# Kernel tuning notes

Measured on AMD Instinct MI355X. Metric: run time of the kernel, lower is better.

Reference implementation:

```python
import jax, jax.numpy as jnp
import numpy as np

CLAMP_MIN = 1e-12
CLAMP_MAX = 1e12


def setup_inputs() -> dict:
    key = jax.random.key(0)
    k1, k2, k3 = jax.random.split(key, 3)
    N, C, H, W = 32, 11, 384, 384
    x = jax.random.normal(k1, (N, C, H, W), dtype=jnp.float32)
    centers = jax.random.normal(k2, (N, C, H, W), dtype=jnp.float32)
    labels = jax.random.randint(k3, (N, H, W), 0, C, dtype=jnp.int64)
    return {"x": x, "centers": centers, "labels": labels}


def reference(x, centers, labels):
    # x, centers: (N, C, H, W); labels: (N, H, W) int
    N, C, H, W = x.shape
    # res[n,c] = x[n,c]^2 + centers[n,c]^2 - 2 * x[n,c] @ centers[n,c]
    # (single batched matmul replaces the original per-(i,j) addmm loop)
    res = x * x + centers * centers - 2.0 * jnp.matmul(x, centers)
    # softmax over class dim, then max over class dim -> (N, H, W)
    res_max = jnp.max(jax.nn.softmax(res, axis=1), axis=1)
    dist = res_max * labels.astype(res_max.dtype)
    loss = jnp.sum(jnp.clip(dist, CLAMP_MIN, CLAMP_MAX)) / (H * W * N)
    return loss
```

## Files before the change

### kernel.cpp

```cpp
#include <hip/hip_runtime.h>
#include <stdint.h>

typedef __attribute__((ext_vector_type(8))) short short8;
typedef __attribute__((ext_vector_type(4))) float floatx4;
typedef __attribute__((ext_vector_type(4))) unsigned short u16x4;

#define Hh 384
#define Ww 384
#define Cc 11
#define Nn 32
#define PITCH 72

__device__ __forceinline__ unsigned short f2bf(float f) {
  union { float f; uint32_t u; } z; z.f = f;
  return (unsigned short)(z.u >> 16);
}
__device__ __forceinline__ float bf2f(unsigned short b) {
  union { uint32_t u; float f; } z; z.u = ((uint32_t)b) << 16;
  return z.f;
}

__global__ __launch_bounds__(256, 3)
void center_loss(const float* __restrict__ X, const float* __restrict__ Cen,
                 const int* __restrict__ Lab, float* __restrict__ Out) {
  __shared__ __align__(16) unsigned short Alds[64 * PITCH];
  __shared__ __align__(16) unsigned short Blds[64 * PITCH];
  __shared__ float red[4];

  const int bx = blockIdx.x;
  const int n  = bx / 36;
  const int t36 = bx - n * 36;
  const int ib = t36 / 6;
  const int jb = t36 - ib * 6;
  const int i0 = ib << 6, j0 = jb << 6;

  const int t   = threadIdx.x;
  const int l   = t & 63;
  const int w   = t >> 6;
  const int wr  = (w >> 1) << 5;
  const int wc  = (w & 1) << 5;
  const int q4  = l >> 4;
  const int l16 = l & 15;
  const int sa  = t & 15;
  const int sr  = t >> 4;

  float m[16], s[16];
#pragma unroll
  for (int i = 0; i < 16; ++i) { m[i] = -3.0e38f; s[i] = 0.0f; }

  for (int c = 0; c < Cc; ++c) {
    const float* xb = X   + (size_t)(n * Cc + c) * (Hh * Ww);
    const float* cb = Cen + (size_t)(n * Cc + c) * (Hh * Ww);

    floatx4 acc[2][2];
#pragma unroll
    for (int a = 0; a < 2; ++a)
#pragma unroll
      for (int b = 0; b < 2; ++b) acc[a][b] = (floatx4){0.f, 0.f, 0.f, 0.f};
    float ev[16];
#pragma unroll
    for (int i = 0; i < 16; ++i) ev[i] = 0.0f;

    for (int kb = 0; kb < 6; ++kb) {
      __syncthreads();
      {
        const float* ap = xb + (size_t)(i0 + sr) * Ww + (kb << 6) + (sa << 2);
#pragma unroll
        for (int p = 0; p < 4; ++p) {
          float4 v = *reinterpret_cast<const float4*>(ap + (size_t)(p * 16) * Ww);
          u16x4 pk;
          pk.x = f2bf(v.x); pk.y = f2bf(v.y); pk.z = f2bf(v.z); pk.w = f2bf(v.w);
          *reinterpret_cast<u16x4*>(&Alds[(sr + 16 * p) * PITCH + (sa << 2)]) = pk;
        }
      }
      {
#pragma unroll
        for (int p = 0; p < 2; ++p) {
          const int kbase = (w << 3) + (p << 5);
          const float* bp = cb + (size_t)((kb << 6) + kbase) * Ww + j0 + l;
          short8 pk;
#pragma unroll
          for (int u = 0; u < 8; ++u) pk[u] = (short)f2bf(bp[(size_t)u * Ww]);
          *reinterpret_cast<short8*>(&Blds[l * PITCH + kbase]) = pk;
        }
      }
      __syncthreads();

      if (kb == jb) {
#pragma unroll
        for (int fr = 0; fr < 2; ++fr)
#pragma unroll
          for (int fc = 0; fc < 2; ++fc)
#pragma unroll
            for (int r = 0; r < 4; ++r) {
              const int idx = ((fr << 1) + fc) * 4 + r;
              const int pr = wr + (fr << 4) + (q4 << 2) + r;
              const int pc = wc + (fc << 4) + l16;
              float xv = bf2f(Alds[pr * PITCH + pc]);
              ev[idx] += xv * xv;
            }
      }
      if (kb == ib) {
#pragma unroll
        for (int fr = 0; fr < 2; ++fr)
#pragma unroll
          for (int fc = 0; fc < 2; ++fc)
#pragma unroll
            for (int r = 0; r < 4; ++r) {
              const int idx = ((fr << 1) + fc) * 4 + r;
              const int pr = wr + (fr << 4) + (q4 << 2) + r;
              const int pc = wc + (fc << 4) + l16;
              float cv = bf2f(Blds[pc * PITCH + pr]);
              ev[idx] += cv * cv;
            }
      }

#pragma unroll
      for (int ks = 0; ks < 2; ++ks) {
        const int ko = (ks << 5) + (q4 << 3);
        short8 a0 = *reinterpret_cast<const short8*>(&Alds[(wr +      l16) * PITCH + ko]);
        short8 a1 = *reinterpret_cast<const short8*>(&Alds[(wr + 16 + l16) * PITCH + ko]);
        short8 b0 = *reinterpret_cast<const short8*>(&Blds[(wc +      l16) * PITCH + ko]);
        short8 b1 = *reinterpret_cast<const short8*>(&Blds[(wc + 16 + l16) * PITCH + ko]);
        acc[0][0] = __builtin_amdgcn_mfma_f32_16x16x32_bf16(a0, b0, acc[0][0], 0, 0, 0);
        acc[0][1] = __builtin_amdgcn_mfma_f32_16x16x32_bf16(a0, b1, acc[0][1], 0, 0, 0);
        acc[1][0] = __builtin_amdgcn_mfma_f32_16x16x32_bf16(a1, b0, acc[1][0], 0, 0, 0);
        acc[1][1] = __builtin_amdgcn_mfma_f32_16x16x32_bf16(a1, b1, acc[1][1], 0, 0, 0);
      }
    }

#pragma unroll
    for (int fr = 0; fr < 2; ++fr)
#pragma unroll
      for (int fc = 0; fc < 2; ++fc)
#pragma unroll
        for (int r = 0; r < 4; ++r) {
          const int idx = ((fr << 1) + fc) * 4 + r;
          float res = ev[idx] - 2.0f * acc[fr][fc][r];
          float mi = m[idx];
          if (res <= mi) {
            s[idx] += __expf(res - mi);
          } else {
            s[idx] = s[idx] * __expf(mi - res) + 1.0f;
            m[idx] = res;
          }
        }
  }

  float local = 0.0f;
  const int* lb = Lab + (size_t)n * (Hh * Ww);
#pragma unroll
  for (int fr = 0; fr < 2; ++fr)
#pragma unroll
    for (int fc = 0; fc < 2; ++fc)
#pragma unroll
      for (int r = 0; r < 4; ++r) {
        const int idx = ((fr << 1) + fc) * 4 + r;
        const int pr = i0 + wr + (fr << 4) + (q4 << 2) + r;
        const int pc = j0 + wc + (fc << 4) + l16;
        float val = 1.0f / s[idx];
        float d = val * (float)lb[pr * Ww + pc];
        d = fminf(fmaxf(d, 1e-12f), 1e12f);
        local += d;
      }
#pragma unroll
  for (int off = 32; off > 0; off >>= 1) local += __shfl_down(local, off, 64);
  if (l == 0) red[w] = local;
  __syncthreads();
  if (t == 0) {
    float bs = (red[0] + red[1] + red[2] + red[3]) * (1.0f / 4718592.0f);
    atomicAdd(Out, bs);
  }
}

extern "C" void kernel_launch(void* const* d_in, const int* in_sizes, int n_in,
                              void* d_out, int out_size, void* d_ws, size_t ws_size,
                              hipStream_t stream) {
  const float* X   = (const float*)d_in[0];
  const float* Cen = (const float*)d_in[1];
  const int*   Lab = (const int*)d_in[2];
  float* Out = (float*)d_out;
  hipMemsetAsync(Out, 0, (size_t)out_size * sizeof(float), stream);
  hipLaunchKernelGGL(center_loss, dim3(Nn * 36), dim3(256), 0, stream,
                     X, Cen, Lab, Out);
}
```

Before: 601.6 us.

## Prefetch next k-tile into registers and remap blocks by XCD

Flattens the channel and k-block loops into one 66-iteration loop. The global loads for the next tile are issued into registers before the compute on the current LDS tile, so memory latency overlaps with MFMA work. Block indices are remapped so that all blocks of one batch item land on the same XCD, which should improve L2 reuse of shared rows and columns. Launch bounds are raised to 4 waves per SIMD. The extra prefetch registers may cause spills or cut real occupancy.

```diff
diff --git a/kernel.cpp b/kernel.cpp
--- a/kernel.cpp
+++ b/kernel.cpp
@@ -20,16 +20,19 @@
   return z.f;
 }
 
-__global__ __launch_bounds__(256, 3)
+__global__ __launch_bounds__(256, 4)
 void center_loss(const float* __restrict__ X, const float* __restrict__ Cen,
                  const int* __restrict__ Lab, float* __restrict__ Out) {
   __shared__ __align__(16) unsigned short Alds[64 * PITCH];
   __shared__ __align__(16) unsigned short Blds[64 * PITCH];
   __shared__ float red[4];
 
-  const int bx = blockIdx.x;
-  const int n  = bx / 36;
-  const int t36 = bx - n * 36;
+  const int bx   = blockIdx.x;
+  const int xcd  = bx & 7;
+  const int slot = bx >> 3;
+  const int grp  = slot / 36;
+  const int t36  = slot - grp * 36;
+  const int n    = xcd + (grp << 3);
   const int ib = t36 / 6;
   const int jb = t36 - ib * 6;
   const int i0 = ib << 6, j0 = jb << 6;
@@ -44,111 +47,154 @@
   const int sa  = t & 15;
   const int sr  = t >> 4;
 
+  const size_t plane = (size_t)Hh * Ww;
+  const float* xbase = X   + (size_t)n * Cc * plane;
+  const float* cbase = Cen + (size_t)n * Cc * plane;
+
   float m[16], s[16];
 #pragma unroll
   for (int i = 0; i < 16; ++i) { m[i] = -3.0e38f; s[i] = 0.0f; }
 
-  for (int c = 0; c < Cc; ++c) {
-    const float* xb = X   + (size_t)(n * Cc + c) * (Hh * Ww);
-    const float* cb = Cen + (size_t)(n * Cc + c) * (Hh * Ww);
-
-    floatx4 acc[2][2];
-#pragma unroll
-    for (int a = 0; a < 2; ++a)
-#pragma unroll
-      for (int b = 0; b < 2; ++b) acc[a][b] = (floatx4){0.f, 0.f, 0.f, 0.f};
-    float ev[16];
-#pragma unroll
-    for (int i = 0; i < 16; ++i) ev[i] = 0.0f;
-
-    for (int kb = 0; kb < 6; ++kb) {
-      __syncthreads();
-      {
-        const float* ap = xb + (size_t)(i0 + sr) * Ww + (kb << 6) + (sa << 2);
-#pragma unroll
-        for (int p = 0; p < 4; ++p) {
-          float4 v = *reinterpret_cast<const float4*>(ap + (size_t)(p * 16) * Ww);
-          u16x4 pk;
-          pk.x = f2bf(v.x); pk.y = f2bf(v.y); pk.z = f2bf(v.z); pk.w = f2bf(v.w);
-          *reinterpret_cast<u16x4*>(&Alds[(sr + 16 * p) * PITCH + (sa << 2)]) = pk;
-        }
+  floatx4 acc[2][2];
+  float ev[16];
+#pragma unroll
+  for (int a = 0; a < 2; ++a)
+#pragma unroll
+    for (int b = 0; b < 2; ++b) acc[a][b] = (floatx4){0.f, 0.f, 0.f, 0.f};
+#pragma unroll
+  for (int i = 0; i < 16; ++i) ev[i] = 0.0f;
+
+  float4 pa[4];
+  float  pb[16];
+
+  {
+    const float* ap = xbase + (size_t)(i0 + sr) * Ww + (sa << 2);
+#pragma unroll
+    for (int p = 0; p < 4; ++p)
+      pa[p] = *reinterpret_cast<const float4*>(ap + (size_t)(p * 16) * Ww);
+#pragma unroll
+    for (int p = 0; p < 2; ++p) {
+      const int kbase = (w << 3) + (p << 5);
+      const float* bp = cbase + (size_t)kbase * Ww + j0 + l;
+#pragma unroll
+      for (int u = 0; u < 8; ++u) pb[p * 8 + u] = bp[(size_t)u * Ww];
+    }
+  }
+
+  int c = 0, kb = 0;
+  for (int it = 0; it < 66; ++it) {
+    __syncthreads();
+
+#pragma unroll
+    for (int p = 0; p < 4; ++p) {
+      u16x4 pk;
+      pk.x = f2bf(pa[p].x); pk.y = f2bf(pa[p].y);
+      pk.z = f2bf(pa[p].z); pk.w = f2bf(pa[p].w);
+      *reinterpret_cast<u16x4*>(&Alds[(sr + 16 * p) * PITCH + (sa << 2)]) = pk;
+    }
+#pragma unroll
+    for (int p = 0; p < 2; ++p) {
+      const int kbase = (w << 3) + (p << 5);
+      short8 pk;
+#pragma unroll
+      for (int u = 0; u < 8; ++u) pk[u] = (short)f2bf(pb[p * 8 + u]);
+      *reinterpret_cast<short8*>(&Blds[l * PITCH + kbase]) = pk;
+    }
+
+    int kn = kb + 1, cn = c;
+    if (kn == 6) { kn = 0; cn = c + 1; }
+    float4 na[4];
+    float  nb[16];
+    if (it < 65) {
+      const float* xb = xbase + (size_t)cn * plane;
+      const float* cb = cbase + (size_t)cn * plane;
+      const float* ap = xb + (size_t)(i0 + sr) * Ww + (kn << 6) + (sa << 2);
+#pragma unroll
+      for (int p = 0; p < 4; ++p)
+        na[p] = *reinterpret_cast<const float4*>(ap + (size_t)(p * 16) * Ww);
+#pragma unroll
+      for (int p = 0; p < 2; ++p) {
+        const int kbase = (w << 3) + (p << 5);
+        const float* bp = cb + (size_t)((kn << 6) + kbase) * Ww + j0 + l;
+#pragma unroll
+        for (int u = 0; u < 8; ++u) nb[p * 8 + u] = bp[(size_t)u * Ww];
       }
-      {
-#pragma unroll
-        for (int p = 0; p < 2; ++p) {
-          const int kbase = (w << 3) + (p << 5);
-          const float* bp = cb + (size_t)((kb << 6) + kbase) * Ww + j0 + l;
-          short8 pk;
-#pragma unroll
-          for (int u = 0; u < 8; ++u) pk[u] = (short)f2bf(bp[(size_t)u * Ww]);
-          *reinterpret_cast<short8*>(&Blds[l * PITCH + kbase]) = pk;
-        }
-      }
-      __syncthreads();
-
-      if (kb == jb) {
-#pragma unroll
-        for (int fr = 0; fr < 2; ++fr)
-#pragma unroll
-          for (int fc = 0; fc < 2; ++fc)
-#pragma unroll
-            for (int r = 0; r < 4; ++r) {
-              const int idx = ((fr << 1) + fc) * 4 + r;
-              const int pr = wr + (fr << 4) + (q4 << 2) + r;
-              const int pc = wc + (fc << 4) + l16;
-              float xv = bf2f(Alds[pr * PITCH + pc]);
-              ev[idx] += xv * xv;
+    }
+
+    __syncthreads();
+
+    if (kb == jb) {
+#pragma unroll
+      for (int fr = 0; fr < 2; ++fr)
+#pragma unroll
+        for (int fc = 0; fc < 2; ++fc)
+#pragma unroll
+          for (int r = 0; r < 4; ++r) {
+            const int idx = ((fr << 1) + fc) * 4 + r;
+            const int pr = wr + (fr << 4) + (q4 << 2) + r;
+            const int pc = wc + (fc << 4) + l16;
+            float xv = bf2f(Alds[pr * PITCH + pc]);
+            ev[idx] += xv * xv;
+          }
+    }
+    if (kb == ib) {
+#pragma unroll
+      for (int fr = 0; fr < 2; ++fr)
+#pragma unroll
+        for (int fc = 0; fc < 2; ++fc)
+#pragma unroll
+          for (int r = 0; r < 4; ++r) {
+            const int idx = ((fr << 1) + fc) * 4 + r;
+            const int pr = wr + (fr << 4) + (q4 << 2) + r;
+            const int pc = wc + (fc << 4) + l16;
+            float cv = bf2f(Blds[pc * PITCH + pr]);
+            ev[idx] += cv * cv;
+          }
+    }
+
+#pragma unroll
+    for (int ks = 0; ks < 2; ++ks) {
+      const int ko = (ks << 5) + (q4 << 3);
+      short8 a0 = *reinterpret_cast<const short8*>(&Alds[(wr +      l16) * PITCH + ko]);
+      short8 a1 = *reinterpret_cast<const short8*>(&Alds[(wr + 16 + l16) * PITCH + ko]);
+      short8 b0 = *reinterpret_cast<const short8*>(&Blds[(wc +      l16) * PITCH + ko]);
+      short8 b1 = *reinterpret_cast<const short8*>(&Blds[(wc + 16 + l16) * PITCH + ko]);
+      acc[0][0] = __builtin_amdgcn_mfma_f32_16x16x32_bf16(a0, b0, acc[0][0], 0, 0, 0);
+      acc[0][1] = __builtin_amdgcn_mfma_f32_16x16x32_bf16(a0, b1, acc[0][1], 0, 0, 0);
+      acc[1][0] = __builtin_amdgcn_mfma_f32_16x16x32_bf16(a1, b0, acc[1][0], 0, 0, 0);
+      acc[1][1] = __builtin_amdgcn_mfma_f32_16x16x32_bf16(a1, b1, acc[1][1], 0, 0, 0);
+    }
+
+    if (kb == 5) {
+#pragma unroll
+      for (int fr = 0; fr < 2; ++fr)
+#pragma unroll
+        for (int fc = 0; fc < 2; ++fc)
+#pragma unroll
+          for (int r = 0; r < 4; ++r) {
+            const int idx = ((fr << 1) + fc) * 4 + r;
+            float res = ev[idx] - 2.0f * acc[fr][fc][r];
+            float mi = m[idx];
+            if (res <= mi) {
+              s[idx] += __expf(res - mi);
+            } else {
+              s[idx] = s[idx] * __expf(mi - res) + 1.0f;
+              m[idx] = res;
             }
-      }
-      if (kb == ib) {
-#pragma unroll
-        for (int fr = 0; fr < 2; ++fr)
-#pragma unroll
-          for (int fc = 0; fc < 2; ++fc)
-#pragma unroll
-            for (int r = 0; r < 4; ++r) {
-              const int idx = ((fr << 1) + fc) * 4 + r;
-              const int pr = wr + (fr << 4) + (q4 << 2) + r;
-              const int pc = wc + (fc << 4) + l16;
-              float cv = bf2f(Blds[pc * PITCH + pr]);
-              ev[idx] += cv * cv;
-            }
-      }
-
-#pragma unroll
-      for (int ks = 0; ks < 2; ++ks) {
-        const int ko = (ks << 5) + (q4 << 3);
-        short8 a0 = *reinterpret_cast<const short8*>(&Alds[(wr +      l16) * PITCH + ko]);
-        short8 a1 = *reinterpret_cast<const short8*>(&Alds[(wr + 16 + l16) * PITCH + ko]);
-        short8 b0 = *reinterpret_cast<const short8*>(&Blds[(wc +      l16) * PITCH + ko]);
-        short8 b1 = *reinterpret_cast<const short8*>(&Blds[(wc + 16 + l16) * PITCH + ko]);
-        acc[0][0] = __builtin_amdgcn_mfma_f32_16x16x32_bf16(a0, b0, acc[0][0], 0, 0, 0);
-        acc[0][1] = __builtin_amdgcn_mfma_f32_16x16x32_bf16(a0, b1, acc[0][1], 0, 0, 0);
-        acc[1][0] = __builtin_amdgcn_mfma_f32_16x16x32_bf16(a1, b0, acc[1][0], 0, 0, 0);
-        acc[1][1] = __builtin_amdgcn_mfma_f32_16x16x32_bf16(a1, b1, acc[1][1], 0, 0, 0);
-      }
-    }
-
-#pragma unroll
-    for (int fr = 0; fr < 2; ++fr)
-#pragma unroll
-      for (int fc = 0; fc < 2; ++fc)
-#pragma unroll
-        for (int r = 0; r < 4; ++r) {
-          const int idx = ((fr << 1) + fc) * 4 + r;
-          float res = ev[idx] - 2.0f * acc[fr][fc][r];
-          float mi = m[idx];
-          if (res <= mi) {
-            s[idx] += __expf(res - mi);
-          } else {
-            s[idx] = s[idx] * __expf(mi - res) + 1.0f;
-            m[idx] = res;
+            acc[fr][fc][r] = 0.0f;
+            ev[idx] = 0.0f;
           }
-        }
+    }
+
+    kb = kn; c = cn;
+#pragma unroll
+    for (int p = 0; p < 4; ++p) pa[p] = na[p];
+#pragma unroll
+    for (int p = 0; p < 16; ++p) pb[p] = nb[p];
   }
 
   float local = 0.0f;
-  const int* lb = Lab + (size_t)n * (Hh * Ww);
+  const int* lb = Lab + (size_t)n * plane;
 #pragma unroll
   for (int fr = 0; fr < 2; ++fr)
 #pragma unroll
```

Result: faster. 494.7 us (-17.8%).
